# Kernel tuning notes

Measured on AMD Instinct MI355X. Metric: run time of the kernel, lower is better.

Reference implementation:

```python
import jax
import jax.numpy as jnp
from jax import lax
import numpy as np

B, C, Wd, Hd = 32, 2048, 7, 7


def setup_inputs() -> dict:
    key = jax.random.key(0)
    k1, k2, k3 = jax.random.split(key, 3)
    x = jax.random.normal(k1, (B, C, Wd, Hd), dtype=jnp.float32)
    # Conv2d(C, C, 3, 1, 1): kaiming-like scale for stability
    conv_w = jax.random.normal(k2, (C, C, 3, 3), dtype=jnp.float32) * (1.0 / np.sqrt(C * 9))
    conv_b = jax.random.normal(k3, (C,), dtype=jnp.float32) * 0.01
    return {"x": x, "conv_w": conv_w, "conv_b": conv_b}


def reference(x, conv_w, conv_b):
    b, c, w, h = x.shape
    n = w * h
    xf = x.reshape(b, c, n)  # [B, C, WH]
    # bilinear channel similarity: [B, C, C]
    bilinear = jnp.einsum('bcn,bdn->bcd', xf, xf) / n
    # softmax over negated similarity along last dim
    W_SCI = jax.nn.softmax(-bilinear, axis=2)
    # attention-weighted channel mix: [B, C, WH]
    Y = jnp.einsum('bcd,bdn->bcn', W_SCI, xf)
    # 3x3 conv, stride 1, padding 1 (SAME)
    Yc = lax.conv_general_dilated(
        Y.reshape(b, c, w, h), conv_w,
        window_strides=(1, 1), padding='SAME',
        dimension_numbers=('NCHW', 'OIHW', 'NCHW'))
    Yc = Yc + conv_b[None, :, None, None]
    Z = Yc.reshape(b, c, n) + xf  # residual
    return Z
```

## Files before the change

### kernel.cpp

```cpp
#include <hip/hip_runtime.h>
#include <stdint.h>

#define BB 32
#define CC 2048
#define NPIX 49
#define KPAD 64

typedef __bf16 bf16;
typedef __bf16 bf16x4 __attribute__((ext_vector_type(4)));
typedef __bf16 bf16x8 __attribute__((ext_vector_type(8)));
typedef float f32x4 __attribute__((ext_vector_type(4)));
typedef uint32_t u32x4 __attribute__((ext_vector_type(4)));
typedef long i64;
typedef long i64x2 __attribute__((ext_vector_type(2)));

#define MFMA(a,b,c) __builtin_amdgcn_mfma_f32_16x16x32_bf16(a,b,c,0,0,0)
#define MFMA8(a,b,c) __builtin_amdgcn_mfma_f32_16x16x32_fp8_fp8(a,b,c,0,0,0)
#define GLOAD_LDS(g, l) __builtin_amdgcn_global_load_lds( \
    (const __attribute__((address_space(1))) void*)(g),   \
    (__attribute__((address_space(3))) void*)(l), 16, 0, 0)

__device__ __forceinline__ uint32_t kperm(uint32_t c) {
    uint32_t local = c & 63u, s = local >> 5, lh = (local >> 3) & 3u, o8 = local & 7u;
    return (c & ~63u) | (lh * 16u + s * 8u + o8);
}

__global__ void prep_fused_kernel(const float* __restrict__ x,
                                  bf16* __restrict__ xb, bf16* __restrict__ xbT) {
    __shared__ float xt[6272];
    const int tid = threadIdx.x;
    const int b = blockIdx.x >> 4, cb = blockIdx.x & 15;
    const float* src = x + ((size_t)(b * 2048 + cb * 128)) * 49;
#pragma unroll
    for (int i = 0; i < 25; i++) {
        int idx = i * 256 + tid;
        if (idx < 6272) xt[idx] = src[idx];
    }
    __syncthreads();
    {
        const int r = tid >> 1, h = tid & 1;
        bf16* dst = xb + ((size_t)(b * 2048 + cb * 128 + r)) * 64 + h * 32;
        const float* row = &xt[r * 49];
#pragma unroll
        for (int v = 0; v < 4; v++) {
            bf16x8 o;
#pragma unroll
            for (int e = 0; e < 8; e++) {
                int n = h * 32 + v * 8 + e;
                o[e] = (bf16)(n < 49 ? row[n] : 0.f);
            }
            *(bf16x8*)(dst + v * 8) = o;
        }
    }
    {
        const int n = tid >> 2, q = tid & 3;
        bf16* dst = xbT + ((size_t)b * 64 + n) * 2048 + cb * 128 + q * 32;
#pragma unroll
        for (int v = 0; v < 4; v++) {
            bf16x8 o;
#pragma unroll
            for (int e = 0; e < 8; e++) {
                int cl = q * 32 + v * 8 + e;
                o[e] = (bf16)(n < 49 ? xt[cl * 49 + n] : 0.f);
            }
            *(bf16x8*)(dst + v * 8) = o;
        }
    }
}

__global__ void castw_wino_kernel(const float* __restrict__ cw, uint8_t* __restrict__ Uw) {
    uint32_t t = blockIdx.x * 256u + threadIdx.x;
    uint32_t q = t & 511u, co = t >> 9;
    uint32_t ci0 = q * 4u;
    uint32_t nci = kperm(ci0);
    const f32x4* src4 = (const f32x4*)(cw + ((size_t)co * 2048u + ci0) * 9u);
    float g[36];
#pragma unroll
    for (int m = 0; m < 9; m++) {
        f32x4 t4 = src4[m];
#pragma unroll
        for (int e = 0; e < 4; e++) g[m * 4 + e] = t4[e];
    }
    float u[16][4];
#pragma unroll
    for (int c4 = 0; c4 < 4; c4++) {
        const float* gg = g + c4 * 9;
        float tr[4][3];
#pragma unroll
        for (int col = 0; col < 3; col++) {
            float a0 = gg[col], a1 = gg[3 + col], a2 = gg[6 + col];
            tr[0][col] = a0;
            tr[1][col] = 0.5f * (a0 + a1 + a2);
            tr[2][col] = 0.5f * (a0 - a1 + a2);
            tr[3][col] = a2;
        }
#pragma unroll
        for (int r = 0; r < 4; r++) {
            u[r * 4 + 0][c4] = tr[r][0];
            u[r * 4 + 1][c4] = 0.5f * (tr[r][0] + tr[r][1] + tr[r][2]);
            u[r * 4 + 2][c4] = 0.5f * (tr[r][0] - tr[r][1] + tr[r][2]);
            u[r * 4 + 3][c4] = tr[r][2];
        }
    }
#pragma unroll
    for (int e = 0; e < 16; e++) {
        int p = __builtin_amdgcn_cvt_pk_fp8_f32(u[e][0] * 16.f, u[e][1] * 16.f, 0, false);
        p = __builtin_amdgcn_cvt_pk_fp8_f32(u[e][2] * 16.f, u[e][3] * 16.f, p, true);
        *(uint32_t*)(Uw + (size_t)e * 4194304u + (size_t)co * 2048u + nci) = (uint32_t)p;
    }
}

__global__ __launch_bounds__(512, 2) void attn_kernel(
    const bf16* __restrict__ xb, const bf16* __restrict__ xbT, uint8_t* __restrict__ Ux)
{
    __shared__ __align__(16) char smem[67584];
    bf16* Ktile = (bf16*)smem;
    bf16* Vtile = (bf16*)(smem + 16384);
    bf16 (*Plds)[16][136] = reinterpret_cast<bf16(*)[16][136]>(smem + 32768);
    bf16 (*Tlds)[132] = reinterpret_cast<bf16(*)[132]>(smem);

    const int tid = threadIdx.x;
    const int w = tid >> 6, l = tid & 63;
    const int lhi = l >> 4, llo = l & 15;
    const uint32_t g = blockIdx.x;
    const int xcd = g & 7, inner = g >> 3;
    const int b = xcd + (inner >> 4) * 8;
    const int cblk = inner & 15;
    const int c0 = cblk * 128 + w * 16;
    const bf16* xbB = xb + (size_t)b * CC * KPAD;
    const bf16* xbTB = xbT + (size_t)b * KPAD * CC;

    bf16x8 aQ[2];
#pragma unroll
    for (int kk = 0; kk < 2; kk++)
        aQ[kk] = *(const bf16x8*)(xbB + (uint32_t)(c0 + llo) * KPAD + kk * 32 + lhi * 8);

    const uint32_t rowK = tid >> 3;
    const uint32_t srcKoff = (uint32_t)(((tid & 7u) ^ (rowK & 7u)) << 3);
    const bf16* kSrc = xbB + (size_t)rowK * KPAD + srcKoff;
    const uint32_t rowV = tid >> 4;
    const uint32_t srcVoff = (uint32_t)(((tid & 15u) ^ (rowV & 7u)) << 3);
    const bf16* vSrc = xbTB + (size_t)rowV * CC + srcVoff;

    f32x4 accY[4];
#pragma unroll
    for (int nf = 0; nf < 4; nf++) accY[nf] = (f32x4){0, 0, 0, 0};
    float rowsum[4] = {};

    const float kES = -0.029442756956917622f;

    for (int dt = 0; dt < 16; dt++) {
        const int d0 = dt * 128;
#pragma unroll
        for (int i = 0; i < 2; i++) {
            GLOAD_LDS(kSrc + (size_t)(d0 + i * 64) * KPAD, (char*)Ktile + i * 8192 + tid * 16);
            GLOAD_LDS(vSrc + d0 + (size_t)i * 32 * CC,     (char*)Vtile + i * 8192 + tid * 16);
        }
        __syncthreads();

        f32x4 accS[8];
#pragma unroll
        for (int df = 0; df < 8; df++) accS[df] = (f32x4){0, 0, 0, 0};
#pragma unroll
        for (int kk = 0; kk < 2; kk++) {
#pragma unroll
            for (int df = 0; df < 8; df++) {
                uint32_t r = (uint32_t)(df * 16 + llo);
                bf16x8 bK = *(const bf16x8*)((const char*)Ktile + r * 128u +
                                             ((((uint32_t)(kk * 4 + lhi)) ^ (r & 7u)) << 4));
                accS[df] = MFMA(aQ[kk], bK, accS[df]);
            }
        }
#pragma unroll
        for (int df = 0; df < 8; df++)
#pragma unroll
            for (int r = 0; r < 4; r++) {
                float p = __builtin_amdgcn_exp2f(accS[df][r] * kES);
                rowsum[r] += p;
                Plds[w][lhi * 4 + r][df * 16 + llo] = (bf16)p;
            }
#pragma unroll
        for (int kk2 = 0; kk2 < 4; kk2++) {
            bf16x8 aP = *(const bf16x8*)&Plds[w][llo][kk2 * 32 + lhi * 8];
#pragma unroll
            for (int nf = 0; nf < 4; nf++) {
                uint32_t r = (uint32_t)(nf * 16 + llo);
                bf16x8 bV = *(const bf16x8*)((const char*)Vtile + r * 256u +
                                             ((((uint32_t)(kk2 * 4 + lhi)) ^ (r & 7u)) << 4));
                accY[nf] = MFMA(aP, bV, accY[nf]);
            }
        }
        __syncthreads();
    }
#pragma unroll
    for (int r = 0; r < 4; r++) {
        float s = rowsum[r];
        s += __shfl_xor(s, 1);
        s += __shfl_xor(s, 2);
        s += __shfl_xor(s, 4);
        s += __shfl_xor(s, 8);
        rowsum[r] = 1.0f / s;
    }
    __syncthreads();
#pragma unroll
    for (int nf = 0; nf < 4; nf++)
#pragma unroll
        for (int r = 0; r < 4; r++) {
            int n = nf * 16 + llo;
            int cl = w * 16 + lhi * 4 + r;
            Tlds[n][cl] = (bf16)(accY[nf][r] * rowsum[r]);
        }
    __syncthreads();

    {
        const int t = tid >> 5;
        const int clg = tid & 31;
        const int cl0 = clg * 4;
        const int ti = t >> 2, tj = t & 3;
        float d[4][4][4];
#pragma unroll
        for (int di = 0; di < 4; di++) {
            int i = 2 * ti + di - 1;
#pragma unroll
            for (int dj = 0; dj < 4; dj++) {
                int j = 2 * tj + dj - 1;
                if (i >= 0 && i < 7 && j >= 0 && j < 7) {
                    bf16x4 v = *(const bf16x4*)&Tlds[i * 7 + j][cl0];
#pragma unroll
                    for (int k = 0; k < 4; k++) d[di][dj][k] = (float)v[k];
                } else {
#pragma unroll
                    for (int k = 0; k < 4; k++) d[di][dj][k] = 0.f;
                }
            }
        }
        float R[4][4][4];
#pragma unroll
        for (int dj = 0; dj < 4; dj++)
#pragma unroll
            for (int k = 0; k < 4; k++) {
                R[0][dj][k] = d[0][dj][k] - d[2][dj][k];
                R[1][dj][k] = d[1][dj][k] + d[2][dj][k];
                R[2][dj][k] = d[2][dj][k] - d[1][dj][k];
                R[3][dj][k] = d[1][dj][k] - d[3][dj][k];
            }
        uint32_t nci = kperm((uint32_t)(cblk * 128 + cl0));
        uint8_t* dst = Ux + (size_t)(b * 16 + t) * 2048 + nci;
#pragma unroll
        for (int r = 0; r < 4; r++) {
            float V[4][4];
#pragma unroll
            for (int k = 0; k < 4; k++) {
                V[0][k] = (R[r][0][k] - R[r][2][k]) * 4.f;
                V[1][k] = (R[r][1][k] + R[r][2][k]) * 4.f;
                V[2][k] = (R[r][2][k] - R[r][1][k]) * 4.f;
                V[3][k] = (R[r][1][k] - R[r][3][k]) * 4.f;
            }
#pragma unroll
            for (int cc = 0; cc < 4; cc++) {
                int p = __builtin_amdgcn_cvt_pk_fp8_f32(V[cc][0], V[cc][1], 0, false);
                p = __builtin_amdgcn_cvt_pk_fp8_f32(V[cc][2], V[cc][3], p, true);
                *(uint32_t*)(dst + (size_t)(r * 4 + cc) * 1048576u) = (uint32_t)p;
            }
        }
    }
}

#define CONV_BARRIER() do { __builtin_amdgcn_sched_barrier(0); \
    __builtin_amdgcn_s_barrier(); __builtin_amdgcn_sched_barrier(0); } while (0)
#define CONV_VMW(n) asm volatile("s_waitcnt vmcnt(" #n ")" ::: "memory")

#define WSTAGE(bufOff, t, kh) do {                                             \
    uint32_t kA_ = (uint32_t)(t) * 128u + (uint32_t)(kh) * 64u;                \
    _Pragma("unroll")                                                          \
    for (int i_ = 0; i_ < 2; i_++) {                                           \
        GLOAD_LDS(srcA[i_] + kA_,                                              \
                  smem + (bufOff) + (kh) * 16384 + i_ * 8192 + tid * 16);      \
        GLOAD_LDS(srcB[i_] + kA_,                                              \
                  smem + (bufOff) + 32768 + (kh) * 16384 + i_ * 8192 + tid * 16); \
    }                                                                          \
} while (0)

#define CONV_PHASE(bufOff, kk, GATE, STAGE_STMT) do {                          \
    CONV_VMW(GATE);                                                            \
    CONV_BARRIER();                                                            \
    i64x2 af[8], bfr[4];                                                       \
    _Pragma("unroll")                                                          \
    for (int f = 0; f < 8; f++)                                                \
        af[f] = *(const i64x2*)(smem + (bufOff) + (kk) * 16384 + offA[f]);     \
    _Pragma("unroll")                                                          \
    for (int f = 0; f < 4; f++)                                                \
        bfr[f] = *(const i64x2*)(smem + (bufOff) + 32768 + (kk) * 16384 + offB[f]); \
    STAGE_STMT;                                                                \
    asm volatile("s_waitcnt lgkmcnt(0)" ::: "memory");                         \
    __builtin_amdgcn_sched_barrier(0);                                         \
    __builtin_amdgcn_s_setprio(1);                                             \
    _Pragma("unroll")                                                          \
    for (int s = 0; s < 2; s++)                                                \
        _Pragma("unroll")                                                      \
        for (int fm = 0; fm < 8; fm++)                                         \
            _Pragma("unroll")                                                  \
            for (int fn = 0; fn < 4; fn++)                                     \
                acc[fm][fn] = MFMA8(af[fm][s], bfr[fn][s], acc[fm][fn]);       \
    __builtin_amdgcn_s_setprio(0);                                             \
    __builtin_amdgcn_sched_barrier(0);                                         \
} while (0)

__global__ __launch_bounds__(512, 2) void wino_gemm_kernel(
    const uint8_t* __restrict__ Ux, const uint8_t* __restrict__ Uw, bf16* __restrict__ Vt)
{
    extern __shared__ __align__(16) char smem[];
    const int tid = threadIdx.x;
    const int w = tid >> 6, l = tid & 63;
    const int lhi = l >> 4, llo = l & 15;
    const int wm = w >> 2, wn = w & 3;

    uint32_t g = blockIdx.x;
    uint32_t xcd = g & 7u, inner = g >> 3;
    uint32_t e = xcd * 2u + (inner >> 4);
    uint32_t sub = inner & 15u;
    uint32_t mt = sub >> 3, nt = sub & 7u;

    uint32_t rowLoc = tid >> 2;
    uint32_t slot = tid & 3u;
    const uint8_t* srcA[2];
    const uint8_t* srcB[2];
#pragma unroll
    for (int i = 0; i < 2; i++) {
        uint32_t row = (uint32_t)i * 128u + rowLoc;
        uint32_t swz = (uint32_t)((slot ^ ((row >> 1) & 3u)) << 4);
        srcA[i] = Ux + (size_t)e * 1048576u + (size_t)(mt * 256u + row) * 2048u + swz;
        srcB[i] = Uw + (size_t)e * 4194304u + (size_t)(nt * 256u + row) * 2048u + swz;
    }

    uint32_t offA[8], offB[4];
#pragma unroll
    for (int f = 0; f < 8; f++) {
        uint32_t r = (uint32_t)(wm * 128 + f * 16 + llo);
        offA[f] = r * 64u + (uint32_t)(((uint32_t)lhi ^ ((r >> 1) & 3u)) << 4);
    }
#pragma unroll
    for (int f = 0; f < 4; f++) {
        uint32_t r = (uint32_t)(wn * 64 + f * 16 + llo);
        offB[f] = r * 64u + (uint32_t)(((uint32_t)lhi ^ ((r >> 1) & 3u)) << 4);
    }

    f32x4 acc[8][4];
#pragma unroll
    for (int fm = 0; fm < 8; fm++)
#pragma unroll
        for (int fn = 0; fn < 4; fn++) acc[fm][fn] = (f32x4){0, 0, 0, 0};

    WSTAGE(0, 0, 0);
    WSTAGE(0, 0, 1);
    WSTAGE(65536, 1, 0);

    for (int it = 0; it < 7; ++it) {
        const int t0 = it * 2;
        CONV_PHASE(0,     0, 8, WSTAGE(65536, t0 + 1, 1));
        CONV_PHASE(0,     1, 8, WSTAGE(0,     t0 + 2, 0));
        CONV_PHASE(65536, 0, 8, WSTAGE(0,     t0 + 2, 1));
        CONV_PHASE(65536, 1, 8, WSTAGE(65536, t0 + 3, 0));
    }
    CONV_PHASE(0,     0, 8, WSTAGE(65536, 15, 1));
    CONV_PHASE(0,     1, 8, (void)0);
    CONV_PHASE(65536, 0, 4, (void)0);
    CONV_PHASE(65536, 1, 0, (void)0);

    bf16* pz = Vt + (size_t)e * 1048576u;
    uint32_t n0 = mt * 256u + (uint32_t)(wm * 128 + lhi * 4);
    uint32_t co0 = nt * 256u + (uint32_t)(wn * 64 + llo);
#pragma unroll
    for (int fm = 0; fm < 8; fm++)
#pragma unroll
        for (int fn = 0; fn < 4; fn++)
#pragma unroll
            for (int r = 0; r < 4; r++)
                pz[(size_t)(n0 + fm * 16u + r) * 2048u + (co0 + fn * 16u)] =
                    (bf16)acc[fm][fn][r];
}

__global__ void wino_out_kernel(const bf16* __restrict__ Vt, const float* __restrict__ x,
                                const float* __restrict__ cb, float* __restrict__ out)
{
    __shared__ float Ml[16][16][33];
    __shared__ float Ol[32][50];
    __shared__ float cbl[32];
    const int tid = threadIdx.x;
    const int b = blockIdx.x >> 6, cg = blockIdx.x & 63;
    const int c0 = cg * 32;

    {
        int e = tid >> 4, t = tid & 15;
        const bf16* src = Vt + ((size_t)e * 512 + b * 16 + t) * 2048 + c0;
#pragma unroll
        for (int v = 0; v < 4; v++) {
            bf16x8 vv = *(const bf16x8*)(src + v * 8);
#pragma unroll
            for (int k = 0; k < 8; k++) Ml[e][t][v * 8 + k] = (float)vv[k] * 0.015625f;
        }
    }
    if (tid < 32) cbl[tid] = cb[c0 + tid];
    __syncthreads();

    {
        int t = tid & 15, cp = tid >> 4;
        int ti = t >> 2, tj = t & 3;
#pragma unroll
        for (int cc2 = 0; cc2 < 2; cc2++) {
            int cc = cp * 2 + cc2;
            float M[16];
#pragma unroll
            for (int e = 0; e < 16; e++) M[e] = Ml[e][t][cc];
            float s0[4], s1[4];
#pragma unroll
            for (int col = 0; col < 4; col++) {
                s0[col] = M[col] + M[4 + col] + M[8 + col];
                s1[col] = M[4 + col] - M[8 + col] - M[12 + col];
            }
            float y00 = s0[0] + s0[1] + s0[2];
            float y01 = s0[1] - s0[2] - s0[3];
            float y10 = s1[0] + s1[1] + s1[2];
            float y11 = s1[1] - s1[2] - s1[3];
            int i0 = 2 * ti, j0 = 2 * tj;
            Ol[cc][i0 * 7 + j0] = y00;
            if (j0 + 1 < 7) Ol[cc][i0 * 7 + j0 + 1] = y01;
            if (i0 + 1 < 7) Ol[cc][(i0 + 1) * 7 + j0] = y10;
            if (i0 + 1 < 7 && j0 + 1 < 7) Ol[cc][(i0 + 1) * 7 + j0 + 1] = y11;
        }
    }
    __syncthreads();

    {
        const float* xs = x + ((size_t)b * 2048 + c0) * 49;
        float* os = out + ((size_t)b * 2048 + c0) * 49;
        for (int k = tid; k < 1568; k += 256) {
            int c = k / 49, p = k - c * 49;
            os[k] = Ol[c][p] + cbl[c] + xs[k];
        }
    }
}

extern "C" void kernel_launch(void* const* d_in, const int* in_sizes, int n_in,
                              void* d_out, int out_size, void* d_ws, size_t ws_size,
                              hipStream_t stream) {
    (void)in_sizes; (void)n_in; (void)out_size; (void)ws_size;
    const float* x = (const float*)d_in[0];
    const float* cw = (const float*)d_in[1];
    const float* cb = (const float*)d_in[2];
    float* out = (float*)d_out;
    char* ws = (char*)d_ws;

    bf16* xb     = (bf16*)(ws);
    bf16* xbT    = (bf16*)(ws + 8388608);
    uint8_t* Ux  = (uint8_t*)(ws + 16777216);
    uint8_t* Uw  = (uint8_t*)(ws + 33554432);
    bf16* Vt     = (bf16*)(ws + 100663296);

    hipFuncSetAttribute((const void*)wino_gemm_kernel,
                        hipFuncAttributeMaxDynamicSharedMemorySize, 131072);

    prep_fused_kernel<<<512, 256, 0, stream>>>(x, xb, xbT);
    castw_wino_kernel<<<4096, 256, 0, stream>>>(cw, Uw);
    attn_kernel<<<512, 512, 0, stream>>>(xb, xbT, Ux);
    wino_gemm_kernel<<<256, 512, 131072, stream>>>(Ux, Uw, Vt);
    wino_out_kernel<<<2048, 256, 0, stream>>>(Vt, x, cb, out);
}
```

Baseline: 185.1 us.

## Switch Winograd GEMM to 16x16x128 scaled FP8 MFMA with natural K layout

The Winograd batched GEMM now uses the gfx950 scaled f8f6f4 MFMA with K=128 per instruction instead of pairs of 16x16x32 fp8 MFMAs. The kperm channel permutation in the weight and input transforms is dropped, and LDS fragment addressing is rewritten so each lane reads 32 contiguous bytes across both K halves. The pipeline stages a full 128-K tile per phase with an extra barrier before restaging, and launch bounds drop to one block per CU. The aim is fewer MFMA issues and higher matrix throughput, at the cost of less load/compute overlap, more register pressure and lower occupancy.

```diff
diff --git a/kernel.cpp b/kernel.cpp
--- a/kernel.cpp
+++ b/kernel.cpp
@@ -11,19 +11,13 @@
 typedef __bf16 bf16x8 __attribute__((ext_vector_type(8)));
 typedef float f32x4 __attribute__((ext_vector_type(4)));
 typedef uint32_t u32x4 __attribute__((ext_vector_type(4)));
-typedef long i64;
 typedef long i64x2 __attribute__((ext_vector_type(2)));
+typedef int i32x8 __attribute__((ext_vector_type(8)));
 
 #define MFMA(a,b,c) __builtin_amdgcn_mfma_f32_16x16x32_bf16(a,b,c,0,0,0)
-#define MFMA8(a,b,c) __builtin_amdgcn_mfma_f32_16x16x32_fp8_fp8(a,b,c,0,0,0)
 #define GLOAD_LDS(g, l) __builtin_amdgcn_global_load_lds( \
     (const __attribute__((address_space(1))) void*)(g),   \
     (__attribute__((address_space(3))) void*)(l), 16, 0, 0)
-
-__device__ __forceinline__ uint32_t kperm(uint32_t c) {
-    uint32_t local = c & 63u, s = local >> 5, lh = (local >> 3) & 3u, o8 = local & 7u;
-    return (c & ~63u) | (lh * 16u + s * 8u + o8);
-}
 
 __global__ void prep_fused_kernel(const float* __restrict__ x,
                                   bf16* __restrict__ xb, bf16* __restrict__ xbT) {
@@ -72,7 +66,6 @@
     uint32_t t = blockIdx.x * 256u + threadIdx.x;
     uint32_t q = t & 511u, co = t >> 9;
     uint32_t ci0 = q * 4u;
-    uint32_t nci = kperm(ci0);
     const f32x4* src4 = (const f32x4*)(cw + ((size_t)co * 2048u + ci0) * 9u);
     float g[36];
 #pragma unroll
@@ -106,7 +99,7 @@
     for (int e = 0; e < 16; e++) {
         int p = __builtin_amdgcn_cvt_pk_fp8_f32(u[e][0] * 16.f, u[e][1] * 16.f, 0, false);
         p = __builtin_amdgcn_cvt_pk_fp8_f32(u[e][2] * 16.f, u[e][3] * 16.f, p, true);
-        *(uint32_t*)(Uw + (size_t)e * 4194304u + (size_t)co * 2048u + nci) = (uint32_t)p;
+        *(uint32_t*)(Uw + (size_t)e * 4194304u + (size_t)co * 2048u + ci0) = (uint32_t)p;
     }
 }
 
@@ -244,8 +237,7 @@
                 R[2][dj][k] = d[2][dj][k] - d[1][dj][k];
                 R[3][dj][k] = d[1][dj][k] - d[3][dj][k];
             }
-        uint32_t nci = kperm((uint32_t)(cblk * 128 + cl0));
-        uint8_t* dst = Ux + (size_t)(b * 16 + t) * 2048 + nci;
+        uint8_t* dst = Ux + (size_t)(b * 16 + t) * 2048 + (uint32_t)(cblk * 128 + cl0);
 #pragma unroll
         for (int r = 0; r < 4; r++) {
             float V[4][4];
@@ -270,43 +262,64 @@
     __builtin_amdgcn_s_barrier(); __builtin_amdgcn_sched_barrier(0); } while (0)
 #define CONV_VMW(n) asm volatile("s_waitcnt vmcnt(" #n ")" ::: "memory")
 
-#define WSTAGE(bufOff, t, kh) do {                                             \
-    uint32_t kA_ = (uint32_t)(t) * 128u + (uint32_t)(kh) * 64u;                \
+#define WSTAGE(bufOff, t) do {                                                 \
     _Pragma("unroll")                                                          \
-    for (int i_ = 0; i_ < 2; i_++) {                                           \
-        GLOAD_LDS(srcA[i_] + kA_,                                              \
-                  smem + (bufOff) + (kh) * 16384 + i_ * 8192 + tid * 16);      \
-        GLOAD_LDS(srcB[i_] + kA_,                                              \
-                  smem + (bufOff) + 32768 + (kh) * 16384 + i_ * 8192 + tid * 16); \
+    for (int kh_ = 0; kh_ < 2; kh_++) {                                        \
+        uint32_t kA_ = (uint32_t)(t) * 128u + (uint32_t)kh_ * 64u;             \
+        _Pragma("unroll")                                                      \
+        for (int i_ = 0; i_ < 2; i_++) {                                       \
+            GLOAD_LDS(srcA[i_] + kA_,                                          \
+                      smem + (bufOff) + kh_ * 16384 + i_ * 8192 + tid * 16);   \
+            GLOAD_LDS(srcB[i_] + kA_,                                          \
+                      smem + (bufOff) + 32768 + kh_ * 16384 + i_ * 8192 + tid * 16); \
+        }                                                                      \
     }                                                                          \
 } while (0)
 
-#define CONV_PHASE(bufOff, kk, GATE, STAGE_STMT) do {                          \
-    CONV_VMW(GATE);                                                            \
-    CONV_BARRIER();                                                            \
-    i64x2 af[8], bfr[4];                                                       \
+#define WPHASE_CORE(bufOff)                                                    \
+    i32x8 af[8]; i32x8 bfr[4];                                                 \
     _Pragma("unroll")                                                          \
-    for (int f = 0; f < 8; f++)                                                \
-        af[f] = *(const i64x2*)(smem + (bufOff) + (kk) * 16384 + offA[f]);     \
+    for (int f = 0; f < 8; f++) {                                              \
+        union { i64x2 h[2]; i32x8 v; } ua_;                                    \
+        ua_.h[0] = *(const i64x2*)(smem + (bufOff) + offA[f]);                 \
+        ua_.h[1] = *(const i64x2*)(smem + (bufOff) + (offA[f] ^ 16u));         \
+        af[f] = ua_.v;                                                         \
+    }                                                                          \
     _Pragma("unroll")                                                          \
-    for (int f = 0; f < 4; f++)                                                \
-        bfr[f] = *(const i64x2*)(smem + (bufOff) + 32768 + (kk) * 16384 + offB[f]); \
-    STAGE_STMT;                                                                \
+    for (int f = 0; f < 4; f++) {                                              \
+        union { i64x2 h[2]; i32x8 v; } ub_;                                    \
+        ub_.h[0] = *(const i64x2*)(smem + (bufOff) + 32768 + offB[f]);         \
+        ub_.h[1] = *(const i64x2*)(smem + (bufOff) + 32768 + (offB[f] ^ 16u)); \
+        bfr[f] = ub_.v;                                                        \
+    }                                                                          \
     asm volatile("s_waitcnt lgkmcnt(0)" ::: "memory");                         \
     __builtin_amdgcn_sched_barrier(0);                                         \
     __builtin_amdgcn_s_setprio(1);                                             \
     _Pragma("unroll")                                                          \
-    for (int s = 0; s < 2; s++)                                                \
+    for (int fm = 0; fm < 8; fm++)                                             \
         _Pragma("unroll")                                                      \
-        for (int fm = 0; fm < 8; fm++)                                         \
-            _Pragma("unroll")                                                  \
-            for (int fn = 0; fn < 4; fn++)                                     \
-                acc[fm][fn] = MFMA8(af[fm][s], bfr[fn][s], acc[fm][fn]);       \
+        for (int fn = 0; fn < 4; fn++)                                         \
+            acc[fm][fn] = __builtin_amdgcn_mfma_scale_f32_16x16x128_f8f6f4(    \
+                af[fm], bfr[fn], acc[fm][fn], 0, 0,                            \
+                0, 0x7F7F7F7F, 0, 0x7F7F7F7F);                                 \
     __builtin_amdgcn_s_setprio(0);                                             \
-    __builtin_amdgcn_sched_barrier(0);                                         \
+    __builtin_amdgcn_sched_barrier(0);
+
+#define WPHASE(bufOff, GATE, STAGE_STMT) do {                                  \
+    CONV_VMW(GATE);                                                            \
+    CONV_BARRIER();                                                            \
+    { WPHASE_CORE(bufOff) }                                                    \
+    CONV_BARRIER();                                                            \
+    STAGE_STMT;                                                                \
 } while (0)
 
-__global__ __launch_bounds__(512, 2) void wino_gemm_kernel(
+#define WPHASE_END(bufOff, GATE) do {                                          \
+    CONV_VMW(GATE);                                                            \
+    CONV_BARRIER();                                                            \
+    { WPHASE_CORE(bufOff) }                                                    \
+} while (0)
+
+__global__ __launch_bounds__(512, 1) void wino_gemm_kernel(
     const uint8_t* __restrict__ Ux, const uint8_t* __restrict__ Uw, bf16* __restrict__ Vt)
 {
     extern __shared__ __align__(16) char smem[];
@@ -337,12 +350,14 @@
 #pragma unroll
     for (int f = 0; f < 8; f++) {
         uint32_t r = (uint32_t)(wm * 128 + f * 16 + llo);
-        offA[f] = r * 64u + (uint32_t)(((uint32_t)lhi ^ ((r >> 1) & 3u)) << 4);
+        offA[f] = (uint32_t)((lhi >> 1) * 16384) + r * 64u +
+                  ((((uint32_t)(2 * (lhi & 1))) ^ ((r >> 1) & 3u)) << 4);
     }
 #pragma unroll
     for (int f = 0; f < 4; f++) {
         uint32_t r = (uint32_t)(wn * 64 + f * 16 + llo);
-        offB[f] = r * 64u + (uint32_t)(((uint32_t)lhi ^ ((r >> 1) & 3u)) << 4);
+        offB[f] = (uint32_t)((lhi >> 1) * 16384) + r * 64u +
+                  ((((uint32_t)(2 * (lhi & 1))) ^ ((r >> 1) & 3u)) << 4);
     }
 
     f32x4 acc[8][4];
@@ -351,21 +366,16 @@
 #pragma unroll
         for (int fn = 0; fn < 4; fn++) acc[fm][fn] = (f32x4){0, 0, 0, 0};
 
-    WSTAGE(0, 0, 0);
-    WSTAGE(0, 0, 1);
-    WSTAGE(65536, 1, 0);
+    WSTAGE(0, 0);
+    WSTAGE(65536, 1);
 
     for (int it = 0; it < 7; ++it) {
         const int t0 = it * 2;
-        CONV_PHASE(0,     0, 8, WSTAGE(65536, t0 + 1, 1));
-        CONV_PHASE(0,     1, 8, WSTAGE(0,     t0 + 2, 0));
-        CONV_PHASE(65536, 0, 8, WSTAGE(0,     t0 + 2, 1));
-        CONV_PHASE(65536, 1, 8, WSTAGE(65536, t0 + 3, 0));
-    }
-    CONV_PHASE(0,     0, 8, WSTAGE(65536, 15, 1));
-    CONV_PHASE(0,     1, 8, (void)0);
-    CONV_PHASE(65536, 0, 4, (void)0);
-    CONV_PHASE(65536, 1, 0, (void)0);
+        WPHASE(0,     8, WSTAGE(0,     t0 + 2));
+        WPHASE(65536, 8, WSTAGE(65536, t0 + 3));
+    }
+    WPHASE_END(0, 8);
+    WPHASE_END(65536, 0);
 
     bf16* pz = Vt + (size_t)e * 1048576u;
     uint32_t n0 = mt * 256u + (uint32_t)(wm * 128 + lhi * 4);
```

After: 248.8 us. 1.34x slower.
